# Optimization experiments

Hardware: AMD Instinct MI355X
Metric: run time of the kernel (lower is better)

## Reference

```python
import jax, jax.numpy as jnp
import numpy as np

GROUP_SIZE = 128
IN_FEATURES = 4096
OUT_FEATURES = 4096
BATCH, SEQ = 4, 2048


def setup_inputs() -> dict:
    key = jax.random.key(0)
    k1, k2, k3, k4 = jax.random.split(key, 4)
    x = jax.random.normal(k1, (BATCH, SEQ, IN_FEATURES), dtype=jnp.float32)
    # packed int4 pairs: values in [0, 256), semantics of uint8
    weight_packed = jax.random.randint(k2, (OUT_FEATURES, IN_FEATURES // 2), 0, 256, dtype=jnp.int32)
    groups = IN_FEATURES // GROUP_SIZE  # 32
    scales = jax.random.uniform(k3, (OUT_FEATURES, groups), dtype=jnp.float32) * 0.02 + 0.001
    zeros = jnp.zeros((OUT_FEATURES, groups), dtype=jnp.float32)  # unused in forward (as in source)
    bias = jax.random.normal(k4, (OUT_FEATURES,), dtype=jnp.float32)
    return {"x": x, "weight_packed": weight_packed, "scales": scales, "zeros": zeros, "bias": bias}


def _unpack_int4(packed, K):
    # low nibble -> even columns, high nibble -> odd columns; values shifted to [-8, 7]
    low = (packed & 15) - 8
    high = ((packed >> 4) & 15) - 8
    M = packed.shape[0]
    return jnp.stack([low, high], axis=-1).reshape(M, K)  # interleave [l0,h0,l1,h1,...]


def reference(x, weight_packed, scales, zeros, bias):
    K = IN_FEATURES
    groups = K // GROUP_SIZE
    w_int = _unpack_int4(weight_packed, K)  # [O, K] int
    w_grouped = w_int.astype(jnp.float32).reshape(OUT_FEATURES, groups, GROUP_SIZE)
    w = (w_grouped * scales[:, :, None]).reshape(OUT_FEATURES, K).astype(x.dtype)
    # F.linear: x @ w^T + bias
    return jnp.einsum('bsk,ok->bso', x, w) + bias
```

## Files before the change

### kernel.cpp

```cpp
#include <hip/hip_runtime.h>
#include <hip/hip_bf16.h>


typedef float f32x4 __attribute__((ext_vector_type(4)));
typedef int   i32x4 __attribute__((ext_vector_type(4)));

#define GAS __attribute__((address_space(1)))
#define LAS __attribute__((address_space(3)))

static constexpr int M_DIM = 8192;
static constexpr int N_DIM = 4096;
static constexpr int K_DIM = 4096;

__global__ __launch_bounds__(256) void quant_x(const float* __restrict__ x,
                                               signed char* __restrict__ xq,
                                               float* __restrict__ sx) {
    const int row = blockIdx.x;
    const int tid = threadIdx.x;
    const float* xr = x + (size_t)row * K_DIM;
    float4 v[4];
#pragma unroll
    for (int i = 0; i < 4; ++i) v[i] = *(const float4*)(xr + i * 1024 + tid * 4);
    float m = 0.f;
#pragma unroll
    for (int i = 0; i < 4; ++i)
        m = fmaxf(m, fmaxf(fmaxf(fabsf(v[i].x), fabsf(v[i].y)),
                           fmaxf(fabsf(v[i].z), fabsf(v[i].w))));
#pragma unroll
    for (int off = 32; off >= 1; off >>= 1) m = fmaxf(m, __shfl_xor(m, off, 64));
    __shared__ float wm[4];
    if ((tid & 63) == 0) wm[tid >> 6] = m;
    __syncthreads();
    m = fmaxf(fmaxf(wm[0], wm[1]), fmaxf(wm[2], wm[3]));
    const float inv = 127.f / m;
    if (tid == 0) sx[row] = m / 127.f;
#pragma unroll
    for (int i = 0; i < 4; ++i) {
        int b0 = (int)rintf(v[i].x * inv) & 255;
        int b1 = (int)rintf(v[i].y * inv) & 255;
        int b2 = (int)rintf(v[i].z * inv) & 255;
        int b3 = (int)rintf(v[i].w * inv) & 255;
        *(int*)(xq + (size_t)row * K_DIM + i * 1024 + tid * 4) =
            b0 | (b1 << 8) | (b2 << 16) | (b3 << 24);
    }
}

__global__ __launch_bounds__(256) void unpack_w(const int* __restrict__ wp,
                                                signed char* __restrict__ wq) {
    const int t = blockIdx.x * 256 + threadIdx.x;
    int4 p = *(const int4*)(wp + (size_t)t * 4);
    int pv[4] = {p.x, p.y, p.z, p.w};
    int w01 = (((pv[0] & 15) - 8) & 255) | (((((pv[0] >> 4) & 15) - 8) & 255) << 8) |
              ((((pv[1] & 15) - 8) & 255) << 16) | (((((pv[1] >> 4) & 15) - 8) & 255) << 24);
    int w23 = (((pv[2] & 15) - 8) & 255) | (((((pv[2] >> 4) & 15) - 8) & 255) << 8) |
              ((((pv[3] & 15) - 8) & 255) << 16) | (((((pv[3] >> 4) & 15) - 8) & 255) << 24);
    *(int2*)(wq + (size_t)t * 8) = make_int2(w01, w23);
}

__global__ __launch_bounds__(256, 3) void gemm_i8(const signed char* __restrict__ A,
                                                  const signed char* __restrict__ B,
                                                  const float* __restrict__ scales,
                                                  const float* __restrict__ sx,
                                                  const float* __restrict__ bias,
                                                  float* __restrict__ C) {
    __shared__ signed char As[128 * 128];
    __shared__ signed char Bs[128 * 128];

    const int tid  = threadIdx.x;
    const int l    = tid & 63;
    const int wv   = tid >> 6;
    const int wr   = wv >> 1;
    const int wc   = wv & 1;
    const int lr   = l & 15;
    const int quad = l >> 4;

    const size_t m0 = (size_t)blockIdx.y * 128;
    const size_t n0 = (size_t)blockIdx.x * 128;

    float accf[4][4][4];
#pragma unroll
    for (int i = 0; i < 4; ++i)
#pragma unroll
        for (int j = 0; j < 4; ++j)
#pragma unroll
            for (int r = 0; r < 4; ++r) accf[i][j][r] = 0.f;

    const i32x4 izero = {0, 0, 0, 0};

    for (int g = 0; g < K_DIM / 128; ++g) {
        const int k0 = g * 128;
        __syncthreads();
#pragma unroll
        for (int q4 = 0; q4 < 4; ++q4) {
            int q   = wv * 4 + q4;
            int s   = q * 64 + l;
            int row = s >> 3;
            int c   = (s & 7) ^ (row & 7);
            const signed char* ga = A + (m0 + row) * K_DIM + k0 + c * 16;
            const signed char* gb = B + (n0 + row) * K_DIM + k0 + c * 16;
            __builtin_amdgcn_global_load_lds((const GAS void*)ga, (LAS void*)(As + q * 1024), 16, 0, 0);
            __builtin_amdgcn_global_load_lds((const GAS void*)gb, (LAS void*)(Bs + q * 1024), 16, 0, 0);
        }
        float sj[4];
#pragma unroll
        for (int j = 0; j < 4; ++j)
            sj[j] = scales[(n0 + (size_t)wc * 64 + j * 16 + lr) * 32 + g];
        __syncthreads();

        i32x4 bf0[4], bf1[4];
#pragma unroll
        for (int j = 0; j < 4; ++j) {
            int row = wc * 64 + j * 16 + lr;
            bf0[j] = *(const i32x4*)(Bs + (row * 8 + (quad ^ (row & 7))) * 16);
            bf1[j] = *(const i32x4*)(Bs + (row * 8 + ((4 + quad) ^ (row & 7))) * 16);
        }
#pragma unroll
        for (int i = 0; i < 4; ++i) {
            int row = wr * 64 + i * 16 + lr;
            i32x4 a0 = *(const i32x4*)(As + (row * 8 + (quad ^ (row & 7))) * 16);
            i32x4 a1 = *(const i32x4*)(As + (row * 8 + ((4 + quad) ^ (row & 7))) * 16);
            i32x4 ci[4];
#pragma unroll
            for (int j = 0; j < 4; ++j)
                ci[j] = __builtin_amdgcn_mfma_i32_16x16x64_i8(a0, bf0[j], izero, 0, 0, 0);
#pragma unroll
            for (int j = 0; j < 4; ++j)
                ci[j] = __builtin_amdgcn_mfma_i32_16x16x64_i8(a1, bf1[j], ci[j], 0, 0, 0);
#pragma unroll
            for (int j = 0; j < 4; ++j)
#pragma unroll
                for (int r = 0; r < 4; ++r)
                    accf[i][j][r] += sj[j] * (float)ci[j][r];
        }
    }

    float sxr[4][4];
#pragma unroll
    for (int i = 0; i < 4; ++i)
#pragma unroll
        for (int r = 0; r < 4; ++r)
            sxr[i][r] = sx[m0 + wr * 64 + i * 16 + quad * 4 + r];
#pragma unroll
    for (int j = 0; j < 4; ++j) {
        int gn   = (int)n0 + wc * 64 + j * 16 + lr;
        float bv = bias[gn];
#pragma unroll
        for (int i = 0; i < 4; ++i) {
            size_t gm = m0 + wr * 64 + i * 16 + quad * 4;
#pragma unroll
            for (int r = 0; r < 4; ++r)
                C[(gm + r) * N_DIM + gn] = accf[i][j][r] * sxr[i][r] + bv;
        }
    }
}

extern "C" void kernel_launch(void* const* d_in, const int* in_sizes, int n_in,
                              void* d_out, int out_size, void* d_ws, size_t ws_size,
                              hipStream_t stream) {
    const float* x      = (const float*)d_in[0];
    const int*   wp     = (const int*)d_in[1];
    const float* scales = (const float*)d_in[2];
    const float* bias   = (const float*)d_in[4];
    float* out = (float*)d_out;

    signed char* Xq = (signed char*)d_ws;
    signed char* Wq = (signed char*)d_ws + (size_t)M_DIM * K_DIM;
    float*       sx = (float*)((char*)d_ws + (size_t)M_DIM * K_DIM + (size_t)N_DIM * K_DIM);

    quant_x<<<M_DIM, 256, 0, stream>>>(x, Xq, sx);
    unpack_w<<<(N_DIM * (K_DIM / 2) / 4) / 256, 256, 0, stream>>>(wp, Wq);
    gemm_i8<<<dim3(N_DIM / 128, M_DIM / 128), 256, 0, stream>>>(Xq, Wq, scales, sx, bias, out);
}
```

Measured before the change: 443.8 us.

## Rewrite int8 GEMM with 256x256 tiles, double-buffered LDS pipeline and XCD-aware mapping

The int8 GEMM now uses 512-thread blocks computing 256x256 output tiles. Operands are double-buffered in 128KB of LDS, with async global-to-LDS loads interleaved between four compute phases per K step and fine-grained vmcnt waits and barriers. Block IDs are remapped so tiles sharing operands land on the same XCD, and MFMA sections are wrapped in s_setprio. A small new kernel transposes the scales so per-group scale loads are contiguous. Together these aim to raise data reuse and hide load latency behind MFMA work, at the cost of more register pressure and tighter barrier ordering.

```diff
diff --git a/kernel.cpp b/kernel.cpp
--- a/kernel.cpp
+++ b/kernel.cpp
@@ -1,9 +1,7 @@
 #include <hip/hip_runtime.h>
-#include <hip/hip_bf16.h>
-
-
-typedef float f32x4 __attribute__((ext_vector_type(4)));
-typedef int   i32x4 __attribute__((ext_vector_type(4)));
+
+
+typedef int i32x4 __attribute__((ext_vector_type(4)));
 
 #define GAS __attribute__((address_space(1)))
 #define LAS __attribute__((address_space(3)))
@@ -57,96 +55,185 @@
     *(int2*)(wq + (size_t)t * 8) = make_int2(w01, w23);
 }
 
-__global__ __launch_bounds__(256, 3) void gemm_i8(const signed char* __restrict__ A,
-                                                  const signed char* __restrict__ B,
-                                                  const float* __restrict__ scales,
+__global__ __launch_bounds__(256) void transp_scales(const float* __restrict__ s,
+                                                     float* __restrict__ st) {
+    const int t = blockIdx.x * 256 + threadIdx.x;
+    st[(size_t)(t & 31) * N_DIM + (t >> 5)] = s[t];
+}
+
+
+#define STAGE_A(BUF, H, TAU) do { \
+  _Pragma("unroll") \
+  for (int r_ = 0; r_ < 2; ++r_) { \
+    const int ra_ = (H) * 64 + wv * 8 + (l >> 3); \
+    const int c_  = (l & 7) ^ (l >> 3); \
+    const signed char* sA_ = Aq + (size_t)(m0 + r_ * 128 + ra_) * K_DIM \
+                                + (size_t)(TAU) * 128 + c_ * 16; \
+    __builtin_amdgcn_global_load_lds((const GAS void*)sA_, \
+        (LAS void*)(lds + ((BUF) * 2 + r_) * 16384 + ((H) * 64 + wv * 8) * 128), 16, 0, 0); \
+  } \
+} while (0)
+
+#define STAGE_B(BUF, H, TAU) do { \
+  _Pragma("unroll") \
+  for (int r_ = 0; r_ < 2; ++r_) { \
+    const int rb_ = (wv >> 2) * 64 + (H) * 32 + (wv & 3) * 8 + (l >> 3); \
+    const int c_  = (l & 7) ^ (l >> 3); \
+    const signed char* sB_ = Bq + (size_t)(n0 + r_ * 128 + rb_) * K_DIM \
+                                + (size_t)(TAU) * 128 + c_ * 16; \
+    __builtin_amdgcn_global_load_lds((const GAS void*)sB_, \
+        (LAS void*)(lds + 65536 + ((BUF) * 2 + r_) * 16384 \
+                    + ((wv >> 2) * 64 + (H) * 32 + (wv & 3) * 8) * 128), 16, 0, 0); \
+  } \
+} while (0)
+
+#define LOAD_SJ(DST, G) do { \
+  _Pragma("unroll") \
+  for (int j_ = 0; j_ < 4; ++j_) \
+    DST[j_] = scalesT[(size_t)(G) * N_DIM + n0 + wc * 64 + j_ * 16 + lr]; \
+} while (0)
+
+#define PHASE(B, MH, NH, S0, S1) do { \
+  i32x4 aF0_[4], aF1_[4], bF0_[2], bF1_[2]; \
+  _Pragma("unroll") \
+  for (int nj = 0; nj < 2; ++nj) { \
+    const int rb = ((wc & 1) << 6) + (NH) * 32 + nj * 16 + lr; \
+    const signed char* bp = lds + 65536 + ((B) * 2 + (wc >> 1)) * 16384 + rb * 128; \
+    bF0_[nj] = *(const i32x4*)(bp + ((quad       ^ (rb & 7)) << 4)); \
+    bF1_[nj] = *(const i32x4*)(bp + (((4 | quad) ^ (rb & 7)) << 4)); \
+  } \
+  _Pragma("unroll") \
+  for (int mi = 0; mi < 4; ++mi) { \
+    const int ra = (MH) * 64 + mi * 16 + lr; \
+    const signed char* ap = lds + ((B) * 2 + wr) * 16384 + ra * 128; \
+    aF0_[mi] = *(const i32x4*)(ap + ((quad       ^ (ra & 7)) << 4)); \
+    aF1_[mi] = *(const i32x4*)(ap + (((4 | quad) ^ (ra & 7)) << 4)); \
+  } \
+  i32x4 ci_[4][2]; \
+  __builtin_amdgcn_s_setprio(1); \
+  _Pragma("unroll") \
+  for (int mi = 0; mi < 4; ++mi) { \
+    ci_[mi][0] = __builtin_amdgcn_mfma_i32_16x16x64_i8(aF0_[mi], bF0_[0], izero, 0, 0, 0); \
+    ci_[mi][1] = __builtin_amdgcn_mfma_i32_16x16x64_i8(aF0_[mi], bF0_[1], izero, 0, 0, 0); \
+  } \
+  _Pragma("unroll") \
+  for (int mi = 0; mi < 4; ++mi) { \
+    ci_[mi][0] = __builtin_amdgcn_mfma_i32_16x16x64_i8(aF1_[mi], bF1_[0], ci_[mi][0], 0, 0, 0); \
+    ci_[mi][1] = __builtin_amdgcn_mfma_i32_16x16x64_i8(aF1_[mi], bF1_[1], ci_[mi][1], 0, 0, 0); \
+  } \
+  __builtin_amdgcn_s_setprio(0); \
+  _Pragma("unroll") \
+  for (int mi = 0; mi < 4; ++mi) \
+    _Pragma("unroll") \
+    for (int r = 0; r < 4; ++r) { \
+      accf[(MH) * 4 + mi][(NH) * 2 + 0][r] += (S0) * (float)ci_[mi][0][r]; \
+      accf[(MH) * 4 + mi][(NH) * 2 + 1][r] += (S1) * (float)ci_[mi][1][r]; \
+    } \
+} while (0)
+
+#define VMW(N) asm volatile("s_waitcnt vmcnt(" #N ")" ::: "memory")
+#define CLB()  asm volatile("" ::: "memory")
+#define BAR()  __builtin_amdgcn_s_barrier()
+
+__global__ __launch_bounds__(512, 2) void gemm_i8(const signed char* __restrict__ Aq,
+                                                  const signed char* __restrict__ Bq,
+                                                  const float* __restrict__ scalesT,
                                                   const float* __restrict__ sx,
                                                   const float* __restrict__ bias,
                                                   float* __restrict__ C) {
-    __shared__ signed char As[128 * 128];
-    __shared__ signed char Bs[128 * 128];
+    __shared__ signed char lds[131072];
 
     const int tid  = threadIdx.x;
     const int l    = tid & 63;
     const int wv   = tid >> 6;
-    const int wr   = wv >> 1;
-    const int wc   = wv & 1;
+    const int wr   = wv >> 2;
+    const int wc   = wv & 3;
     const int lr   = l & 15;
     const int quad = l >> 4;
 
-    const size_t m0 = (size_t)blockIdx.y * 128;
-    const size_t n0 = (size_t)blockIdx.x * 128;
-
-    float accf[4][4][4];
-#pragma unroll
-    for (int i = 0; i < 4; ++i)
+    const int bid = blockIdx.x;
+    const int xcd = bid & 7, kk = bid >> 3;
+    const int bx = (xcd & 1) * 8 + (kk & 7);
+    const int by = (xcd >> 1) * 8 + (kk >> 3);
+    const int m0 = by * 256, n0 = bx * 256;
+
+    float accf[8][4][4];
+#pragma unroll
+    for (int i = 0; i < 8; ++i)
 #pragma unroll
         for (int j = 0; j < 4; ++j)
 #pragma unroll
             for (int r = 0; r < 4; ++r) accf[i][j][r] = 0.f;
 
     const i32x4 izero = {0, 0, 0, 0};
-
-    for (int g = 0; g < K_DIM / 128; ++g) {
-        const int k0 = g * 128;
-        __syncthreads();
-#pragma unroll
-        for (int q4 = 0; q4 < 4; ++q4) {
-            int q   = wv * 4 + q4;
-            int s   = q * 64 + l;
-            int row = s >> 3;
-            int c   = (s & 7) ^ (row & 7);
-            const signed char* ga = A + (m0 + row) * K_DIM + k0 + c * 16;
-            const signed char* gb = B + (n0 + row) * K_DIM + k0 + c * 16;
-            __builtin_amdgcn_global_load_lds((const GAS void*)ga, (LAS void*)(As + q * 1024), 16, 0, 0);
-            __builtin_amdgcn_global_load_lds((const GAS void*)gb, (LAS void*)(Bs + q * 1024), 16, 0, 0);
-        }
-        float sj[4];
-#pragma unroll
-        for (int j = 0; j < 4; ++j)
-            sj[j] = scales[(n0 + (size_t)wc * 64 + j * 16 + lr) * 32 + g];
-        __syncthreads();
-
-        i32x4 bf0[4], bf1[4];
-#pragma unroll
-        for (int j = 0; j < 4; ++j) {
-            int row = wc * 64 + j * 16 + lr;
-            bf0[j] = *(const i32x4*)(Bs + (row * 8 + (quad ^ (row & 7))) * 16);
-            bf1[j] = *(const i32x4*)(Bs + (row * 8 + ((4 + quad) ^ (row & 7))) * 16);
-        }
-#pragma unroll
-        for (int i = 0; i < 4; ++i) {
-            int row = wr * 64 + i * 16 + lr;
-            i32x4 a0 = *(const i32x4*)(As + (row * 8 + (quad ^ (row & 7))) * 16);
-            i32x4 a1 = *(const i32x4*)(As + (row * 8 + ((4 + quad) ^ (row & 7))) * 16);
-            i32x4 ci[4];
-#pragma unroll
-            for (int j = 0; j < 4; ++j)
-                ci[j] = __builtin_amdgcn_mfma_i32_16x16x64_i8(a0, bf0[j], izero, 0, 0, 0);
-#pragma unroll
-            for (int j = 0; j < 4; ++j)
-                ci[j] = __builtin_amdgcn_mfma_i32_16x16x64_i8(a1, bf1[j], ci[j], 0, 0, 0);
-#pragma unroll
-            for (int j = 0; j < 4; ++j)
-#pragma unroll
-                for (int r = 0; r < 4; ++r)
-                    accf[i][j][r] += sj[j] * (float)ci[j][r];
-        }
+    float sjc0[4], sjc1[4], sjn0[4], sjn1[4];
+
+    LOAD_SJ(sjc0, 0);
+    LOAD_SJ(sjc1, 1);
+    STAGE_A(0, 0, 0);
+    STAGE_B(0, 0, 0);
+    STAGE_B(0, 1, 0);
+    STAGE_A(0, 1, 0);
+    VMW(4);
+    BAR();
+
+#pragma unroll 1
+    for (int it = 0; it < 16; ++it) {
+        const int t1  = it * 2 + 1;
+        const int tn0 = (it * 2 + 2) & 31;
+        const int tn1 = (it * 2 + 3) & 31;
+
+        STAGE_A(1, 0, t1); LOAD_SJ(sjn0, tn0);
+        PHASE(0, 0, 0, sjc0[0], sjc0[1]);
+        VMW(8); BAR();
+
+        STAGE_B(1, 0, t1);
+        PHASE(0, 0, 1, sjc0[2], sjc0[3]);
+        VMW(8); BAR();
+
+        STAGE_B(1, 1, t1);
+        PHASE(0, 1, 0, sjc0[0], sjc0[1]);
+        CLB(); BAR();
+
+        STAGE_A(1, 1, t1);
+        PHASE(0, 1, 1, sjc0[2], sjc0[3]);
+        VMW(4); BAR();
+
+        STAGE_A(0, 0, tn0); LOAD_SJ(sjn1, tn1);
+        PHASE(1, 0, 0, sjc1[0], sjc1[1]);
+        VMW(8); BAR();
+
+        STAGE_B(0, 0, tn0);
+        PHASE(1, 0, 1, sjc1[2], sjc1[3]);
+        VMW(8); BAR();
+
+        STAGE_B(0, 1, tn0);
+        PHASE(1, 1, 0, sjc1[0], sjc1[1]);
+        CLB(); BAR();
+
+        STAGE_A(0, 1, tn0);
+        PHASE(1, 1, 1, sjc1[2], sjc1[3]);
+        VMW(4); BAR();
+
+#pragma unroll
+        for (int j = 0; j < 4; ++j) { sjc0[j] = sjn0[j]; sjc1[j] = sjn1[j]; }
     }
 
-    float sxr[4][4];
-#pragma unroll
-    for (int i = 0; i < 4; ++i)
+    asm volatile("s_waitcnt vmcnt(0)" ::: "memory");
+
+    float sxr[8][4];
+#pragma unroll
+    for (int i = 0; i < 8; ++i)
 #pragma unroll
         for (int r = 0; r < 4; ++r)
-            sxr[i][r] = sx[m0 + wr * 64 + i * 16 + quad * 4 + r];
+            sxr[i][r] = sx[m0 + wr * 128 + i * 16 + quad * 4 + r];
 #pragma unroll
     for (int j = 0; j < 4; ++j) {
-        int gn   = (int)n0 + wc * 64 + j * 16 + lr;
-        float bv = bias[gn];
-#pragma unroll
-        for (int i = 0; i < 4; ++i) {
-            size_t gm = m0 + wr * 64 + i * 16 + quad * 4;
+        const int gn = n0 + wc * 64 + j * 16 + lr;
+        const float bv = bias[gn];
+#pragma unroll
+        for (int i = 0; i < 8; ++i) {
+            const size_t gm = (size_t)m0 + wr * 128 + i * 16 + quad * 4;
 #pragma unroll
             for (int r = 0; r < 4; ++r)
                 C[(gm + r) * N_DIM + gn] = accf[i][j][r] * sxr[i][r] + bv;
@@ -165,9 +252,11 @@
 
     signed char* Xq = (signed char*)d_ws;
     signed char* Wq = (signed char*)d_ws + (size_t)M_DIM * K_DIM;
-    float*       sx = (float*)((char*)d_ws + (size_t)M_DIM * K_DIM + (size_t)N_DIM * K_DIM);
+    float* sx  = (float*)((char*)d_ws + (size_t)M_DIM * K_DIM + (size_t)N_DIM * K_DIM);
+    float* scT = (float*)((char*)d_ws + (size_t)M_DIM * K_DIM + (size_t)N_DIM * K_DIM + 32768);
 
     quant_x<<<M_DIM, 256, 0, stream>>>(x, Xq, sx);
     unpack_w<<<(N_DIM * (K_DIM / 2) / 4) / 256, 256, 0, stream>>>(wp, Wq);
-    gemm_i8<<<dim3(N_DIM / 128, M_DIM / 128), 256, 0, stream>>>(Xq, Wq, scales, sx, bias, out);
-}
+    transp_scales<<<(N_DIM * 32) / 256, 256, 0, stream>>>(scales, scT);
+    gemm_i8<<<dim3(512), 512, 0, stream>>>(Xq, Wq, scT, sx, bias, out);
+}
```

Result: slower. 1.172 ms (+164.1%).

## Triple-buffer int8 GEMM with 256x128 tiles, 16 waves and XCD-aware tile mapping

Applied to the files above, without the earlier changes.

Rewrites the int8 GEMM to use 1024-thread blocks computing 256x128 output tiles. The K loop is software-pipelined with a three-slot LDS ring and fine-grained vmcnt waits, so global-to-LDS loads run ahead of the MFMA work. Blocks are remapped so neighbouring tiles share an XCD for L2 reuse, and MFMA sections are raised with s_setprio. A small extra kernel transposes the group scales so each k-group reads them contiguously. In exchange, about 144KB of LDS per block limits each CU to a single block, and the last iterations issue harmless wrap-around prefetches.

```diff
diff --git a/kernel.cpp b/kernel.cpp
--- a/kernel.cpp
+++ b/kernel.cpp
@@ -1,9 +1,7 @@
 #include <hip/hip_runtime.h>
-#include <hip/hip_bf16.h>
-
-
-typedef float f32x4 __attribute__((ext_vector_type(4)));
-typedef int   i32x4 __attribute__((ext_vector_type(4)));
+
+
+typedef int i32x4 __attribute__((ext_vector_type(4)));
 
 #define GAS __attribute__((address_space(1)))
 #define LAS __attribute__((address_space(3)))
@@ -57,82 +55,128 @@
     *(int2*)(wq + (size_t)t * 8) = make_int2(w01, w23);
 }
 
-__global__ __launch_bounds__(256, 3) void gemm_i8(const signed char* __restrict__ A,
-                                                  const signed char* __restrict__ B,
-                                                  const float* __restrict__ scales,
-                                                  const float* __restrict__ sx,
-                                                  const float* __restrict__ bias,
-                                                  float* __restrict__ C) {
-    __shared__ signed char As[128 * 128];
-    __shared__ signed char Bs[128 * 128];
+__global__ __launch_bounds__(256) void transp_scales(const float* __restrict__ s,
+                                                     float* __restrict__ st) {
+    const int t = blockIdx.x * 256 + threadIdx.x;
+    st[(size_t)(t & 31) * N_DIM + (t >> 5)] = s[t];
+}
+
+
+#define STAGE(SLOT, TAU) do { \
+  _Pragma("unroll") \
+  for (int i_ = 0; i_ < 2; ++i_) { \
+    const int ch_ = i_ * 1024 + tid; \
+    const int row_ = ch_ >> 3; \
+    const int c_ = (ch_ & 7) ^ (row_ & 7); \
+    const signed char* sA_ = Aq + (size_t)(m0 + row_) * K_DIM \
+                                + (size_t)(TAU) * 128 + c_ * 16; \
+    __builtin_amdgcn_global_load_lds((const GAS void*)sA_, \
+        (LAS void*)(lds + (SLOT) * 49152 + ch_ * 16), 16, 0, 0); \
+  } \
+  { \
+    const int row_ = tid >> 3; \
+    const int c_ = (tid & 7) ^ (row_ & 7); \
+    const signed char* sB_ = Bq + (size_t)(n0 + row_) * K_DIM \
+                                + (size_t)(TAU) * 128 + c_ * 16; \
+    __builtin_amdgcn_global_load_lds((const GAS void*)sB_, \
+        (LAS void*)(lds + (SLOT) * 49152 + 32768 + tid * 16), 16, 0, 0); \
+  } \
+} while (0)
+
+#define VMW(N) asm volatile("s_waitcnt vmcnt(" #N ")" ::: "memory")
+#define BAR()  do { __builtin_amdgcn_s_barrier(); asm volatile("" ::: "memory"); } while (0)
+
+__global__ __launch_bounds__(1024, 4)
+void gemm_i8(const signed char* __restrict__ Aq,
+             const signed char* __restrict__ Bq,
+             const float* __restrict__ scalesT,
+             const float* __restrict__ sx,
+             const float* __restrict__ bias,
+             float* __restrict__ C) {
+    __shared__ signed char lds[147456];
 
     const int tid  = threadIdx.x;
     const int l    = tid & 63;
     const int wv   = tid >> 6;
-    const int wr   = wv >> 1;
-    const int wc   = wv & 1;
+    const int wr   = wv >> 2;
+    const int wc   = wv & 3;
     const int lr   = l & 15;
     const int quad = l >> 4;
 
-    const size_t m0 = (size_t)blockIdx.y * 128;
-    const size_t n0 = (size_t)blockIdx.x * 128;
-
-    float accf[4][4][4];
+    const int bid = blockIdx.x;
+    const int xcd = bid & 7, kk = bid >> 3;
+    const int by = (xcd >> 1) * 8 + (kk & 7);
+    const int bx = (xcd & 1) * 16 + (kk >> 3);
+    const int m0 = by * 256, n0 = bx * 128;
+
+    float accf[4][2][4];
 #pragma unroll
     for (int i = 0; i < 4; ++i)
 #pragma unroll
-        for (int j = 0; j < 4; ++j)
+        for (int j = 0; j < 2; ++j)
 #pragma unroll
             for (int r = 0; r < 4; ++r) accf[i][j][r] = 0.f;
 
     const i32x4 izero = {0, 0, 0, 0};
 
-    for (int g = 0; g < K_DIM / 128; ++g) {
-        const int k0 = g * 128;
-        __syncthreads();
-#pragma unroll
-        for (int q4 = 0; q4 < 4; ++q4) {
-            int q   = wv * 4 + q4;
-            int s   = q * 64 + l;
-            int row = s >> 3;
-            int c   = (s & 7) ^ (row & 7);
-            const signed char* ga = A + (m0 + row) * K_DIM + k0 + c * 16;
-            const signed char* gb = B + (n0 + row) * K_DIM + k0 + c * 16;
-            __builtin_amdgcn_global_load_lds((const GAS void*)ga, (LAS void*)(As + q * 1024), 16, 0, 0);
-            __builtin_amdgcn_global_load_lds((const GAS void*)gb, (LAS void*)(Bs + q * 1024), 16, 0, 0);
+    STAGE(0, 0);
+    STAGE(1, 1);
+    VMW(3);
+    BAR();
+
+#pragma unroll 1
+    for (int t = 0; t < 32; ++t) {
+        const int slot = t % 3;
+        const int sl2  = (t + 2) % 3;
+        const int tau2 = (t + 2) & 31;
+
+        float sj0 = scalesT[(size_t)t * N_DIM + n0 + wc * 32 + lr];
+        float sj1 = scalesT[(size_t)t * N_DIM + n0 + wc * 32 + 16 + lr];
+
+        STAGE(sl2, tau2);
+
+        const signed char* abase = lds + slot * 49152;
+        const signed char* bbase = abase + 32768;
+
+        i32x4 ci[4][2];
+#pragma unroll
+        for (int ks = 0; ks < 2; ++ks) {
+            i32x4 bF[2], aF[4];
+#pragma unroll
+            for (int nj = 0; nj < 2; ++nj) {
+                const int rb = wc * 32 + nj * 16 + lr;
+                bF[nj] = *(const i32x4*)(bbase + rb * 128 +
+                                         ((((ks << 2) | quad) ^ (rb & 7)) << 4));
+            }
+#pragma unroll
+            for (int mi = 0; mi < 4; ++mi) {
+                const int ra = wr * 64 + mi * 16 + lr;
+                aF[mi] = *(const i32x4*)(abase + ra * 128 +
+                                         ((((ks << 2) | quad) ^ (ra & 7)) << 4));
+            }
+            __builtin_amdgcn_s_setprio(1);
+#pragma unroll
+            for (int mi = 0; mi < 4; ++mi)
+#pragma unroll
+                for (int nj = 0; nj < 2; ++nj)
+                    ci[mi][nj] = __builtin_amdgcn_mfma_i32_16x16x64_i8(
+                        aF[mi], bF[nj], ks ? ci[mi][nj] : izero, 0, 0, 0);
+            __builtin_amdgcn_s_setprio(0);
         }
-        float sj[4];
-#pragma unroll
-        for (int j = 0; j < 4; ++j)
-            sj[j] = scales[(n0 + (size_t)wc * 64 + j * 16 + lr) * 32 + g];
-        __syncthreads();
-
-        i32x4 bf0[4], bf1[4];
-#pragma unroll
-        for (int j = 0; j < 4; ++j) {
-            int row = wc * 64 + j * 16 + lr;
-            bf0[j] = *(const i32x4*)(Bs + (row * 8 + (quad ^ (row & 7))) * 16);
-            bf1[j] = *(const i32x4*)(Bs + (row * 8 + ((4 + quad) ^ (row & 7))) * 16);
-        }
-#pragma unroll
-        for (int i = 0; i < 4; ++i) {
-            int row = wr * 64 + i * 16 + lr;
-            i32x4 a0 = *(const i32x4*)(As + (row * 8 + (quad ^ (row & 7))) * 16);
-            i32x4 a1 = *(const i32x4*)(As + (row * 8 + ((4 + quad) ^ (row & 7))) * 16);
-            i32x4 ci[4];
-#pragma unroll
-            for (int j = 0; j < 4; ++j)
-                ci[j] = __builtin_amdgcn_mfma_i32_16x16x64_i8(a0, bf0[j], izero, 0, 0, 0);
-#pragma unroll
-            for (int j = 0; j < 4; ++j)
-                ci[j] = __builtin_amdgcn_mfma_i32_16x16x64_i8(a1, bf1[j], ci[j], 0, 0, 0);
-#pragma unroll
-            for (int j = 0; j < 4; ++j)
-#pragma unroll
-                for (int r = 0; r < 4; ++r)
-                    accf[i][j][r] += sj[j] * (float)ci[j][r];
-        }
+
+#pragma unroll
+        for (int mi = 0; mi < 4; ++mi)
+#pragma unroll
+            for (int r = 0; r < 4; ++r) {
+                accf[mi][0][r] += sj0 * (float)ci[mi][0][r];
+                accf[mi][1][r] += sj1 * (float)ci[mi][1][r];
+            }
+
+        VMW(3);
+        BAR();
     }
+
+    asm volatile("s_waitcnt vmcnt(0)" ::: "memory");
 
     float sxr[4][4];
 #pragma unroll
@@ -141,12 +185,12 @@
         for (int r = 0; r < 4; ++r)
             sxr[i][r] = sx[m0 + wr * 64 + i * 16 + quad * 4 + r];
 #pragma unroll
-    for (int j = 0; j < 4; ++j) {
-        int gn   = (int)n0 + wc * 64 + j * 16 + lr;
-        float bv = bias[gn];
+    for (int j = 0; j < 2; ++j) {
+        const int gn = n0 + wc * 32 + j * 16 + lr;
+        const float bv = bias[gn];
 #pragma unroll
         for (int i = 0; i < 4; ++i) {
-            size_t gm = m0 + wr * 64 + i * 16 + quad * 4;
+            const size_t gm = (size_t)m0 + wr * 64 + i * 16 + quad * 4;
 #pragma unroll
             for (int r = 0; r < 4; ++r)
                 C[(gm + r) * N_DIM + gn] = accf[i][j][r] * sxr[i][r] + bv;
@@ -165,9 +209,11 @@
 
     signed char* Xq = (signed char*)d_ws;
     signed char* Wq = (signed char*)d_ws + (size_t)M_DIM * K_DIM;
-    float*       sx = (float*)((char*)d_ws + (size_t)M_DIM * K_DIM + (size_t)N_DIM * K_DIM);
+    float* sx  = (float*)((char*)d_ws + (size_t)M_DIM * K_DIM + (size_t)N_DIM * K_DIM);
+    float* scT = (float*)((char*)d_ws + (size_t)M_DIM * K_DIM + (size_t)N_DIM * K_DIM + 32768);
 
     quant_x<<<M_DIM, 256, 0, stream>>>(x, Xq, sx);
     unpack_w<<<(N_DIM * (K_DIM / 2) / 4) / 256, 256, 0, stream>>>(wp, Wq);
-    gemm_i8<<<dim3(N_DIM / 128, M_DIM / 128), 256, 0, stream>>>(Xq, Wq, scales, sx, bias, out);
-}
+    transp_scales<<<(N_DIM * 32) / 256, 256, 0, stream>>>(scales, scT);
+    gemm_i8<<<dim3(1024), 1024, 0, stream>>>(Xq, Wq, scT, sx, bias, out);
+}
```

After: 429.1 us. -3.3%, faster.
